# Kernel tuning notes

Measured on AMD Instinct MI355X. Metric: run time of the kernel, lower is better.

Reference implementation:

```python
import jax, jax.numpy as jnp
import numpy as np

D_MODEL = 1024
N_HEADS = 16
D_HEAD = D_MODEL // N_HEADS


def setup_inputs() -> dict:
    key = jax.random.key(0)
    k1, k2, k3 = jax.random.split(key, 3)
    x = jax.random.normal(k1, (4, 2048, D_MODEL), dtype=jnp.float32)
    # torch Linear(d, 3d, bias=False): y = x @ W.T with W [3d, d].
    # We store the transposed form W_qkv [d, 3d] so y = x @ W_qkv (same math).
    scale = 1.0 / np.sqrt(D_MODEL)
    W_qkv = jax.random.normal(k2, (D_MODEL, 3 * D_MODEL), dtype=jnp.float32) * scale
    W_o = jax.random.normal(k3, (D_MODEL, D_MODEL), dtype=jnp.float32) * scale
    return {"x": x, "W_qkv": W_qkv, "W_o": W_o}


def reference(x, W_qkv, W_o):
    B, T, C = x.shape
    qkv = x @ W_qkv                              # [B, T, 3C]
    Q, K, V = jnp.split(qkv, 3, axis=-1)
    def to_heads(t):
        return t.reshape(B, T, N_HEADS, D_HEAD).transpose(0, 2, 1, 3)  # [B,H,T,d]
    Q, K, V = to_heads(Q), to_heads(K), to_heads(V)
    scores = jnp.einsum("bhqd,bhkd->bhqk", Q, K) / np.sqrt(D_HEAD)
    attn = jax.nn.softmax(scores, axis=-1)
    # dropout is identity in eval/deterministic mode
    context = jnp.einsum("bhqk,bhkd->bhqd", attn, V)
    context = context.transpose(0, 2, 1, 3).reshape(B, T, C)
    return context @ W_o
```

## Files before the change

### kernel.cpp

```cpp
#include <hip/hip_runtime.h>
#include <hip/hip_bf16.h>

typedef __attribute__((ext_vector_type(8))) short short8;
typedef __attribute__((ext_vector_type(4))) float f32x4;
typedef __attribute__((ext_vector_type(16))) float f32x16;
typedef __attribute__((ext_vector_type(2))) unsigned int uint2v;
typedef __attribute__((ext_vector_type(4))) unsigned int uint4v;

#define SEQ    2048
#define DM     1024
#define NH     16
#define DH     64
#define NBATCH 4
#define MTOK   (NBATCH * SEQ)
#define SEG    ((size_t)NBATCH * NH * SEQ * DH)
#define QSCALE 0.18033688f

static __device__ __forceinline__ unsigned bfbits(float f) {
  unsigned u = __float_as_uint(f);
  return u + 0x7fffu + ((u >> 16) & 1u);
}
static __device__ __forceinline__ unsigned short f2bf(float f) {
  return (unsigned short)(bfbits(f) >> 16);
}
static __device__ __forceinline__ unsigned pack2bf(float lo, float hi) {
  return __builtin_amdgcn_perm(bfbits(hi), bfbits(lo), 0x07060302u);
}
static __device__ __forceinline__ unsigned pack2tr(unsigned ulo, unsigned uhi) {
  return __builtin_amdgcn_perm(uhi, ulo, 0x07060302u);
}

typedef const __attribute__((address_space(1))) unsigned int* gp_t;
typedef __attribute__((address_space(3))) unsigned int* lp_t;
static __device__ __forceinline__ void gload_lds16(const void* g, void* l) {
  __builtin_amdgcn_global_load_lds((gp_t)g, (lp_t)l, 16, 0, 0);
}

__global__ __launch_bounds__(256) void xcast(const float* __restrict__ x,
                                             unsigned short* __restrict__ xb) {
  size_t i = ((size_t)blockIdx.x * 256 + threadIdx.x) * 8;
  f32x4 a = *(const f32x4*)&x[i];
  f32x4 b = *(const f32x4*)&x[i + 4];
  uint4v s;
  s[0] = pack2bf(a[0], a[1]);
  s[1] = pack2bf(a[2], a[3]);
  s[2] = pack2bf(b[0], b[1]);
  s[3] = pack2bf(b[2], b[3]);
  *(uint4v*)&xb[i] = s;
}

__global__ __launch_bounds__(256) void transpose_w(
    const float* __restrict__ W, unsigned short* __restrict__ WT, int K, int N) {
  __shared__ float T[64][65];
  const int tid = threadIdx.x;
  const int n0 = blockIdx.x * 64;
  const int k0 = blockIdx.y * 64;
#pragma unroll
  for (int it = 0; it < 4; it++) {
    int row = it * 16 + (tid >> 4);
    int c4 = (tid & 15) * 4;
    f32x4 v = *(const f32x4*)&W[(size_t)(k0 + row) * N + n0 + c4];
#pragma unroll
    for (int j = 0; j < 4; j++) T[row][c4 + j] = v[j];
  }
  __syncthreads();
#pragma unroll
  for (int it = 0; it < 2; it++) {
    int chunk = tid + it * 256;
    int n = chunk >> 3;
    int c8 = (chunk & 7) * 8;
    uint4v s;
#pragma unroll
    for (int j = 0; j < 4; j++)
      s[j] = pack2bf(T[c8 + 2 * j][n], T[c8 + 2 * j + 1][n]);
    *(uint4v*)&WT[(size_t)(n0 + n) * K + k0 + c8] = s;
  }
}

template <int MODE>
__global__ __launch_bounds__(256) void gemm_kernel(
    const void* __restrict__ Av, const unsigned short* __restrict__ BT,
    unsigned short* __restrict__ out0, unsigned short* __restrict__ out1,
    unsigned short* __restrict__ out2, float* __restrict__ outf,
    int M, int N, int K) {
  __shared__ unsigned short As[128][64];
  __shared__ unsigned short Bs[128][64];

  const int tid = threadIdx.x;
  const int wave = tid >> 6;
  const int lane = tid & 63;
  const int quad = lane >> 4;
  const int lc = lane & 15;
  const int wr = wave >> 1;
  const int wc = wave & 1;
  const int m0 = blockIdx.y * 128;
  const int n0 = blockIdx.x * 128;
  const int xsw = lc & 7;
  const int lr8 = lane >> 3;
  const int sgo = ((lane & 7) ^ (lr8 & 7)) * 8;

  f32x4 acc[4][4];
#pragma unroll
  for (int i = 0; i < 4; i++)
#pragma unroll
    for (int j = 0; j < 4; j++) acc[i][j] = (f32x4){0.f, 0.f, 0.f, 0.f};

  for (int k0 = 0; k0 < K; k0 += 64) {
    if (MODE == 0) {
      const float* A = (const float*)Av;
#pragma unroll
      for (int i = 0; i < 4; i++) {
        int chunk = tid + i * 256;
        int r = chunk >> 3;
        int g = chunk & 7;
        int scol = (g ^ (r & 7)) * 8;
        f32x4 v0 = *(const f32x4*)&A[(size_t)(m0 + r) * K + k0 + scol];
        f32x4 v1 = *(const f32x4*)&A[(size_t)(m0 + r) * K + k0 + scol + 4];
        uint4v s;
        s[0] = pack2bf(v0[0], v0[1]);
        s[1] = pack2bf(v0[2], v0[3]);
        s[2] = pack2bf(v1[0], v1[1]);
        s[3] = pack2bf(v1[2], v1[3]);
        *(uint4v*)&As[r][g * 8] = s;
      }
    } else {
      const unsigned short* A = (const unsigned short*)Av;
#pragma unroll
      for (int it = 0; it < 4; it++) {
        int rbase = wave * 32 + it * 8;
        gload_lds16(&A[(size_t)(m0 + rbase + lr8) * K + k0 + sgo],
                    &As[rbase][0]);
      }
    }
#pragma unroll
    for (int it = 0; it < 4; it++) {
      int rbase = wave * 32 + it * 8;
      gload_lds16(&BT[(size_t)(n0 + rbase + lr8) * K + k0 + sgo],
                  &Bs[rbase][0]);
    }
    __syncthreads();

#pragma unroll
    for (int kc = 0; kc < 2; kc++) {
      short8 aA[4], bB[4];
#pragma unroll
      for (int mt = 0; mt < 4; mt++)
        aA[mt] = *(const short8*)&As[wr * 64 + mt * 16 + lc]
                                    [((kc * 4 + quad) ^ xsw) * 8];
#pragma unroll
      for (int nt = 0; nt < 4; nt++)
        bB[nt] = *(const short8*)&Bs[wc * 64 + nt * 16 + lc]
                                    [((kc * 4 + quad) ^ xsw) * 8];
#pragma unroll
      for (int mt = 0; mt < 4; mt++)
#pragma unroll
        for (int nt = 0; nt < 4; nt++)
          acc[mt][nt] = __builtin_amdgcn_mfma_f32_16x16x32_bf16(
              aA[mt], bB[nt], acc[mt][nt], 0, 0, 0);
    }
    __syncthreads();
  }

  const int c = n0 >> 10;
#pragma unroll
  for (int mt = 0; mt < 4; mt++)
#pragma unroll
    for (int nt = 0; nt < 4; nt++) {
      int rb = m0 + wr * 64 + mt * 16 + quad * 4;
      int col = n0 + wc * 64 + nt * 16 + lc;
      if (MODE == 1) {
#pragma unroll
        for (int r = 0; r < 4; r++)
          outf[(size_t)(rb + r) * N + col] = acc[mt][nt][r];
      } else {
        int rem = col & 1023;
        int h = rem >> 6;
        int dd = rem & 63;
        int b = rb >> 11;
        int tt = rb & 2047;
        if (c == 2) {
          uint2v pk;
          pk[0] = pack2bf(acc[mt][nt][0], acc[mt][nt][1]);
          pk[1] = pack2bf(acc[mt][nt][2], acc[mt][nt][3]);
          *(uint2v*)&out2[(((size_t)(b * NH + h)) * DH + dd) * SEQ + tt] = pk;
        } else {
          unsigned short* dst = (c == 0) ? out0 : out1;
          float sc = (c == 0) ? QSCALE : 1.0f;
#pragma unroll
          for (int r = 0; r < 4; r++)
            dst[(((size_t)(b * NH + h) * SEQ + tt + r) << 6) + dd] =
                f2bf(acc[mt][nt][r] * sc);
        }
      }
    }
}

__global__ __launch_bounds__(256) void attn_kernel(
    const unsigned short* __restrict__ Q, const unsigned short* __restrict__ K,
    const unsigned short* __restrict__ Vt, unsigned short* __restrict__ ctx) {
  __shared__ unsigned short KsL[64 * 64];
  __shared__ unsigned short VtL[64 * 64];
  __shared__ unsigned short Ps[4][32][68];
  __shared__ float lbuf[4][32];

  const int tid = threadIdx.x;
  const int wave = tid >> 6;
  const int lane = tid & 63;
  const int half = lane >> 5;
  const int l31 = lane & 31;
  const int bh = blockIdx.y;
  const int q0 = blockIdx.x * 128 + wave * 32;
  const size_t kqbase = (size_t)bh * SEQ * DH;
  const size_t vbase = (size_t)bh * DH * SEQ;

  short8 bQ[4];
#pragma unroll
  for (int dc = 0; dc < 4; dc++)
    bQ[dc] = *(const short8*)&Q[kqbase + (size_t)(q0 + l31) * DH + dc * 16 + half * 8];

  f32x16 o[2];
#pragma unroll
  for (int nb = 0; nb < 2; nb++)
#pragma unroll
    for (int j = 0; j < 16; j++) o[nb][j] = 0.f;
  float l_part = 0.f;

  const int xsw = l31 & 7;
  const int g0 = wave * 128 + lane;
  const int r0 = g0 >> 3, r1 = (g0 + 64) >> 3;
  const size_t so0 = (size_t)r0 * DH + (((g0 & 7) ^ (r0 & 7)) * 8);
  const size_t so1 = (size_t)r1 * DH + (((g0 & 7) ^ (r1 & 7)) * 8);
  const size_t sv0 = (size_t)r0 * SEQ + (((g0 & 7) ^ (r0 & 7)) * 8);
  const size_t sv1 = (size_t)r1 * SEQ + (((g0 & 7) ^ (r1 & 7)) * 8);
  unsigned short* ksl0 = &KsL[(size_t)(wave * 128) * 8];
  unsigned short* ksl1 = &KsL[(size_t)(wave * 128 + 64) * 8];
  unsigned short* vtl0 = &VtL[(size_t)(wave * 128) * 8];
  unsigned short* vtl1 = &VtL[(size_t)(wave * 128 + 64) * 8];

  for (int kt = 0; kt < SEQ / 64; kt++) {
    const size_t kg = kqbase + (size_t)kt * 64 * DH;
    const size_t vg = vbase + (size_t)kt * 64;
    gload_lds16(&K[kg + so0], ksl0);
    gload_lds16(&K[kg + so1], ksl1);
    gload_lds16(&Vt[vg + sv0], vtl0);
    gload_lds16(&Vt[vg + sv1], vtl1);
    __syncthreads();

#pragma unroll
    for (int kb = 0; kb < 2; kb++) {
      f32x16 s;
#pragma unroll
      for (int j = 0; j < 16; j++) s[j] = 0.f;
#pragma unroll
      for (int dc = 0; dc < 4; dc++) {
        const short8 aK = *(const short8*)&KsL[(size_t)(kb * 32 + l31) * 64 +
                                               ((dc * 2 + half) ^ xsw) * 8];
        s = __builtin_amdgcn_mfma_f32_32x32x16_bf16(aK, bQ[dc], s, 0, 0, 0);
      }
#pragma unroll
      for (int gq = 0; gq < 4; gq++) {
        unsigned u0 = __float_as_uint(__builtin_amdgcn_exp2f(s[gq * 4 + 0]));
        unsigned u1 = __float_as_uint(__builtin_amdgcn_exp2f(s[gq * 4 + 1]));
        unsigned u2 = __float_as_uint(__builtin_amdgcn_exp2f(s[gq * 4 + 2]));
        unsigned u3 = __float_as_uint(__builtin_amdgcn_exp2f(s[gq * 4 + 3]));
        float t0 = __uint_as_float(u0 & 0xffff0000u);
        float t1 = __uint_as_float(u1 & 0xffff0000u);
        float t2 = __uint_as_float(u2 & 0xffff0000u);
        float t3 = __uint_as_float(u3 & 0xffff0000u);
        l_part += (t0 + t1) + (t2 + t3);
        uint2v pk;
        pk[0] = pack2tr(u0, u1);
        pk[1] = pack2tr(u2, u3);
        *(uint2v*)&Ps[wave][l31][kb * 32 + gq * 8 + half * 4] = pk;
      }
    }

#pragma unroll
    for (int kc = 0; kc < 4; kc++) {
      uint2v plo = *(const uint2v*)&Ps[wave][l31][kc * 16 + half * 8];
      uint2v phi = *(const uint2v*)&Ps[wave][l31][kc * 16 + half * 8 + 4];
      union { unsigned u[4]; short8 s8; } cv;
      cv.u[0] = plo[0]; cv.u[1] = plo[1]; cv.u[2] = phi[0]; cv.u[3] = phi[1];
      const short8 pA = cv.s8;
#pragma unroll
      for (int nb = 0; nb < 2; nb++) {
        const short8 bV = *(const short8*)&VtL[(size_t)(nb * 32 + l31) * 64 +
                                               ((kc * 2 + half) ^ xsw) * 8];
        o[nb] = __builtin_amdgcn_mfma_f32_32x32x16_bf16(pA, bV, o[nb], 0, 0, 0);
      }
    }
    __syncthreads();
  }

  l_part += __shfl_xor(l_part, 32);
  lbuf[wave][l31] = 1.0f / l_part;
  __syncthreads();

  const int b = bh >> 4;
  const int h = bh & 15;
#pragma unroll
  for (int gq = 0; gq < 4; gq++)
#pragma unroll
    for (int j = 0; j < 4; j++) {
      int ql = j + gq * 8 + half * 4;
      float inv = lbuf[wave][ql];
      int token = blockIdx.x * 128 + wave * 32 + ql;
#pragma unroll
      for (int nb = 0; nb < 2; nb++)
        ctx[((size_t)b * SEQ + token) * DM + h * DH + nb * 32 + l31] =
            f2bf(o[nb][gq * 4 + j] * inv);
    }
}

extern "C" void kernel_launch(void* const* d_in, const int* in_sizes, int n_in,
                              void* d_out, int out_size, void* d_ws,
                              size_t ws_size, hipStream_t stream) {
  const float* x = (const float*)d_in[0];
  const float* Wqkv = (const float*)d_in[1];
  const float* Wo = (const float*)d_in[2];
  float* out = (float*)d_out;
  unsigned short* ws = (unsigned short*)d_ws;

  unsigned short* Qb = ws;
  unsigned short* Kb = ws + SEG;
  unsigned short* Vt = ws + 2 * SEG;
  unsigned short* Ctx = ws + 3 * SEG;
  unsigned short* WqT = Ctx + (size_t)MTOK * DM;
  unsigned short* WoT = WqT + (size_t)3 * DM * DM;
  unsigned short* Xb = WoT + (size_t)DM * DM;
  const size_t need =
      ((size_t)(Xb - ws) + (size_t)MTOK * DM) * sizeof(unsigned short);

  transpose_w<<<dim3(3 * DM / 64, DM / 64), 256, 0, stream>>>(Wqkv, WqT, DM, 3 * DM);
  transpose_w<<<dim3(DM / 64, DM / 64), 256, 0, stream>>>(Wo, WoT, DM, DM);

  if (ws_size >= need) {
    xcast<<<(MTOK * DM) / (256 * 8), 256, 0, stream>>>(x, Xb);
    gemm_kernel<2><<<dim3(3 * DM / 128, MTOK / 128), 256, 0, stream>>>(
        (const void*)Xb, WqT, Qb, Kb, Vt, nullptr, MTOK, 3 * DM, DM);
  } else {
    gemm_kernel<0><<<dim3(3 * DM / 128, MTOK / 128), 256, 0, stream>>>(
        (const void*)x, WqT, Qb, Kb, Vt, nullptr, MTOK, 3 * DM, DM);
  }
  attn_kernel<<<dim3(SEQ / 128, NBATCH * NH), 256, 0, stream>>>(Qb, Kb, Vt, Ctx);
  gemm_kernel<1><<<dim3(DM / 128, MTOK / 128), 256, 0, stream>>>(
      (const void*)Ctx, WoT, nullptr, nullptr, nullptr, out, MTOK, DM, DM);
}
```

Baseline: 281.3 us.

## Double-buffer K/V tiles and keep P in registers via permlane32 swap

Splits the K and V shared-memory tiles into two buffers so the next tile's global-to-LDS load is issued before computing on the current one, overlapping loads with MFMA work. The P matrix no longer round-trips through an LDS scratch array; lanes exchange halves with v_permlane32_swap to form the MFMA A operand directly. It also raises wave priority around the MFMA sections. The cost is double the K/V shared memory, which may lower occupancy. Correctness depends on the single end-of-loop barrier preventing the prefetch from overwriting a buffer other waves are still reading.

```diff
diff --git a/kernel.cpp b/kernel.cpp
--- a/kernel.cpp
+++ b/kernel.cpp
@@ -198,9 +198,8 @@
 __global__ __launch_bounds__(256) void attn_kernel(
     const unsigned short* __restrict__ Q, const unsigned short* __restrict__ K,
     const unsigned short* __restrict__ Vt, unsigned short* __restrict__ ctx) {
-  __shared__ unsigned short KsL[64 * 64];
-  __shared__ unsigned short VtL[64 * 64];
-  __shared__ unsigned short Ps[4][32][68];
+  __shared__ unsigned short KsL[2][64 * 64];
+  __shared__ unsigned short VtL[2][64 * 64];
   __shared__ float lbuf[4][32];
 
   const int tid = threadIdx.x;
@@ -232,31 +231,43 @@
   const size_t so1 = (size_t)r1 * DH + (((g0 & 7) ^ (r1 & 7)) * 8);
   const size_t sv0 = (size_t)r0 * SEQ + (((g0 & 7) ^ (r0 & 7)) * 8);
   const size_t sv1 = (size_t)r1 * SEQ + (((g0 & 7) ^ (r1 & 7)) * 8);
-  unsigned short* ksl0 = &KsL[(size_t)(wave * 128) * 8];
-  unsigned short* ksl1 = &KsL[(size_t)(wave * 128 + 64) * 8];
-  unsigned short* vtl0 = &VtL[(size_t)(wave * 128) * 8];
-  unsigned short* vtl1 = &VtL[(size_t)(wave * 128 + 64) * 8];
-
-  for (int kt = 0; kt < SEQ / 64; kt++) {
+  const int ldo = wave * 1024;
+
+  auto stage = [&](int kt, int b) {
     const size_t kg = kqbase + (size_t)kt * 64 * DH;
     const size_t vg = vbase + (size_t)kt * 64;
-    gload_lds16(&K[kg + so0], ksl0);
-    gload_lds16(&K[kg + so1], ksl1);
-    gload_lds16(&Vt[vg + sv0], vtl0);
-    gload_lds16(&Vt[vg + sv1], vtl1);
-    __syncthreads();
+    unsigned short* kd = &KsL[b][ldo];
+    unsigned short* vd = &VtL[b][ldo];
+    gload_lds16(&K[kg + so0], kd);
+    gload_lds16(&K[kg + so1], kd + 512);
+    gload_lds16(&Vt[vg + sv0], vd);
+    gload_lds16(&Vt[vg + sv1], vd + 512);
+  };
+
+  stage(0, 0);
+  __syncthreads();
+
+  for (int kt = 0; kt < SEQ / 64; kt++) {
+    const int cur = kt & 1;
+    if (kt + 1 < SEQ / 64) stage(kt + 1, cur ^ 1);
+    const unsigned short* kcur = &KsL[cur][0];
+    const unsigned short* vcur = &VtL[cur][0];
 
 #pragma unroll
     for (int kb = 0; kb < 2; kb++) {
       f32x16 s;
 #pragma unroll
       for (int j = 0; j < 16; j++) s[j] = 0.f;
+      __builtin_amdgcn_s_setprio(1);
 #pragma unroll
       for (int dc = 0; dc < 4; dc++) {
-        const short8 aK = *(const short8*)&KsL[(size_t)(kb * 32 + l31) * 64 +
-                                               ((dc * 2 + half) ^ xsw) * 8];
+        const short8 aK = *(const short8*)&kcur[(size_t)(kb * 32 + l31) * 64 +
+                                                ((dc * 2 + half) ^ xsw) * 8];
         s = __builtin_amdgcn_mfma_f32_32x32x16_bf16(aK, bQ[dc], s, 0, 0, 0);
       }
+      __builtin_amdgcn_s_setprio(0);
+
+      unsigned d0[4], d1[4];
 #pragma unroll
       for (int gq = 0; gq < 4; gq++) {
         unsigned u0 = __float_as_uint(__builtin_amdgcn_exp2f(s[gq * 4 + 0]));
@@ -268,25 +279,27 @@
         float t2 = __uint_as_float(u2 & 0xffff0000u);
         float t3 = __uint_as_float(u3 & 0xffff0000u);
         l_part += (t0 + t1) + (t2 + t3);
-        uint2v pk;
-        pk[0] = pack2tr(u0, u1);
-        pk[1] = pack2tr(u2, u3);
-        *(uint2v*)&Ps[wave][l31][kb * 32 + gq * 8 + half * 4] = pk;
-      }
-    }
-
-#pragma unroll
-    for (int kc = 0; kc < 4; kc++) {
-      uint2v plo = *(const uint2v*)&Ps[wave][l31][kc * 16 + half * 8];
-      uint2v phi = *(const uint2v*)&Ps[wave][l31][kc * 16 + half * 8 + 4];
-      union { unsigned u[4]; short8 s8; } cv;
-      cv.u[0] = plo[0]; cv.u[1] = plo[1]; cv.u[2] = phi[0]; cv.u[3] = phi[1];
-      const short8 pA = cv.s8;
-#pragma unroll
-      for (int nb = 0; nb < 2; nb++) {
-        const short8 bV = *(const short8*)&VtL[(size_t)(nb * 32 + l31) * 64 +
-                                               ((kc * 2 + half) ^ xsw) * 8];
-        o[nb] = __builtin_amdgcn_mfma_f32_32x32x16_bf16(pA, bV, o[nb], 0, 0, 0);
+        d0[gq] = pack2tr(u0, u1);
+        d1[gq] = pack2tr(u2, u3);
+      }
+
+#pragma unroll
+      for (int kcl = 0; kcl < 2; kcl++) {
+        unsigned w0 = d0[kcl * 2], w2 = d0[kcl * 2 + 1];
+        unsigned w1 = d1[kcl * 2], w3 = d1[kcl * 2 + 1];
+        asm("v_permlane32_swap_b32 %0, %1" : "+v"(w0), "+v"(w2));
+        asm("v_permlane32_swap_b32 %0, %1" : "+v"(w1), "+v"(w3));
+        union { unsigned u[4]; short8 s8; } cv;
+        cv.u[0] = w0; cv.u[1] = w1; cv.u[2] = w2; cv.u[3] = w3;
+        const int kc = kb * 2 + kcl;
+        __builtin_amdgcn_s_setprio(1);
+#pragma unroll
+        for (int nb = 0; nb < 2; nb++) {
+          const short8 bV = *(const short8*)&vcur[(size_t)(nb * 32 + l31) * 64 +
+                                                  ((kc * 2 + half) ^ xsw) * 8];
+          o[nb] = __builtin_amdgcn_mfma_f32_32x32x16_bf16(cv.s8, bV, o[nb], 0, 0, 0);
+        }
+        __builtin_amdgcn_s_setprio(0);
       }
     }
     __syncthreads();
```

After: 288.9 us. +2.7%, slower.
